# Kernel optimization log

Hardware: AMD Instinct MI355X
Metric: run time of the kernel (lower is better)

The kernel has to match this reference:

```python
import jax, jax.numpy as jnp
import numpy as np

N = 100000      # nodes
E = 1600000     # edges (before self-loops)
IN = 128        # in_dim
HID = 128       # hidden_dim
H = 4           # heads
D = HID // H    # head_dim = 32
L = 3           # n_layers
G = 128         # graphs in batch
NEG_SLOPE = 0.2 # PyG GATConv default leaky_relu slope
BN_EPS = 1e-5


def setup_inputs() -> dict:
    key = jax.random.key(0)
    ks = jax.random.split(key, 16)
    x = jax.random.normal(ks[0], (N, IN), dtype=jnp.float32)
    edge_index = jax.random.randint(ks[1], (2, E), 0, N, dtype=jnp.int64)
    batch = jnp.sort(jax.random.randint(ks[2], (N,), 0, G, dtype=jnp.int64))
    # stacked per-layer GATConv params (in_dim == hidden_dim so all layers stack)
    W = jax.random.normal(ks[3], (L, HID, HID), dtype=jnp.float32) * (1.0 / np.sqrt(HID))
    att_src = jax.random.normal(ks[4], (L, H, D), dtype=jnp.float32) * 0.1
    att_dst = jax.random.normal(ks[5], (L, H, D), dtype=jnp.float32) * 0.1
    bias = jax.random.normal(ks[6], (L, HID), dtype=jnp.float32) * 0.01
    # BatchNorm1d (eval mode: running stats)
    gamma = 1.0 + 0.1 * jax.random.normal(ks[7], (L, HID), dtype=jnp.float32)
    beta = 0.01 * jax.random.normal(ks[8], (L, HID), dtype=jnp.float32)
    bn_mean = jnp.zeros((L, HID), dtype=jnp.float32)
    bn_var = jnp.ones((L, HID), dtype=jnp.float32)
    # MLP head: Linear(HID, HID//2) -> ReLU -> Linear(HID//2, 1)
    Wh1 = jax.random.normal(ks[9], (HID, HID // 2), dtype=jnp.float32) * (1.0 / np.sqrt(HID))
    bh1 = jnp.zeros((HID // 2,), dtype=jnp.float32)
    Wh2 = jax.random.normal(ks[10], (HID // 2, 1), dtype=jnp.float32) * (1.0 / np.sqrt(HID // 2))
    bh2 = jnp.zeros((1,), dtype=jnp.float32)
    return {"x": x, "edge_index": edge_index, "batch": batch, "W": W,
            "att_src": att_src, "att_dst": att_dst, "bias": bias,
            "gamma": gamma, "beta": beta, "bn_mean": bn_mean, "bn_var": bn_var,
            "Wh1": Wh1, "bh1": bh1, "Wh2": Wh2, "bh2": bh2}


def _gat_conv(x, src, dst, W_l, asrc, adst, b):
    # x: [N, F_in]; src/dst: [E+N] (self-loops included); returns [N, H*D]
    h = (x @ W_l).reshape(N, H, D)                      # [N,H,D]
    a_s = jnp.einsum('nhd,hd->nh', h, asrc)             # [N,H]
    a_d = jnp.einsum('nhd,hd->nh', h, adst)
    e = jax.nn.leaky_relu(a_s[src] + a_d[dst], NEG_SLOPE)  # [Etot,H]
    # segment softmax over incoming edges per destination node
    e_max = jax.ops.segment_max(e, dst, num_segments=N)    # [N,H]
    p = jnp.exp(e - e_max[dst])
    denom = jax.ops.segment_sum(p, dst, num_segments=N)    # [N,H]
    alpha = p / (denom[dst] + 1e-16)                        # [Etot,H]
    msg = h[src] * alpha[:, :, None]                        # [Etot,H,D]
    out = jax.ops.segment_sum(msg, dst, num_segments=N)     # [N,H,D]
    return out.reshape(N, H * D) + b


def reference(x, edge_index, batch, W, att_src, att_dst, bias,
              gamma, beta, bn_mean, bn_var, Wh1, bh1, Wh2, bh2):
    # add self-loops once (PyG GATConv default add_self_loops=True)
    loop = jnp.arange(N, dtype=edge_index.dtype)
    src = jnp.concatenate([edge_index[0], loop])
    dst = jnp.concatenate([edge_index[1], loop])
    for l in range(L):
        x = _gat_conv(x, src, dst, W[l], att_src[l], att_dst[l], bias[l])
        x = jnp.maximum(x, 0.0)
        # BatchNorm1d, eval mode (dropout is identity in eval)
        x = (x - bn_mean[l]) * (gamma[l] / jnp.sqrt(bn_var[l] + BN_EPS)) + beta[l]
    # global mean pool over graphs
    sums = jax.ops.segment_sum(x, batch, num_segments=G)            # [G,HID]
    cnts = jax.ops.segment_sum(jnp.ones((N,), x.dtype), batch, num_segments=G)
    pooled = sums / jnp.maximum(cnts, 1.0)[:, None]
    hdn = jnp.maximum(pooled @ Wh1 + bh1, 0.0)
    return (hdn @ Wh2 + bh2).squeeze(-1)                            # [G]
```

## Files before the change

### kernel.cpp

```cpp
#include <hip/hip_runtime.h>
#include <hip/hip_fp16.h>


typedef __bf16 bf16x8 __attribute__((ext_vector_type(8)));
typedef float  f32x4  __attribute__((ext_vector_type(4)));
typedef unsigned int u32x4 __attribute__((ext_vector_type(4)));

#define BCOLS 144
#define BSTRIDE (BCOLS * 128)

#define MAXBKT 800
#define BCAP   4096

__global__ __launch_bounds__(256)
void k_bucket(const int* __restrict__ ei, unsigned int* __restrict__ bkt,
              int* __restrict__ bcnt, float* __restrict__ gsum,
              int* __restrict__ gcnt, int Ne, int Nn, int nbkt, int Gg) {
    __shared__ int lcnt[MAXBKT];
    __shared__ int lbase[MAXBKT];
    int tid = threadIdx.x;
    int gid = blockIdx.x * 256 + tid;
    if (gid < Gg * 128) gsum[gid] = 0.f;
    if (gid < Gg) gcnt[gid] = 0;
    for (int i = tid; i < nbkt; i += 256) lcnt[i] = 0;
    __syncthreads();
    int chunk0 = blockIdx.x * 2048;
    int nnz = Ne + Nn;
    for (int i = 0; i < 8; ++i) {
        int e = chunk0 + i * 256 + tid;
        if (e < nnz) {
            int d = (e < Ne) ? ei[Ne + e] : (e - Ne);
            atomicAdd(&lcnt[d >> 7], 1);
        }
    }
    __syncthreads();
    for (int b = tid; b < nbkt; b += 256) {
        int c = lcnt[b];
        lbase[b] = (c > 0) ? atomicAdd(&bcnt[b], c) : 0;
        lcnt[b] = 0;
    }
    __syncthreads();
    for (int i = 0; i < 8; ++i) {
        int e = chunk0 + i * 256 + tid;
        if (e < nnz) {
            int s, d;
            if (e < Ne) { s = ei[e]; d = ei[Ne + e]; }
            else        { s = e - Ne; d = e - Ne; }
            int b = d >> 7;
            int r = atomicAdd(&lcnt[b], 1);
            bkt[(long)b * BCAP + lbase[b] + r] = ((unsigned)s << 7) | (unsigned)(d & 127);
        }
    }
}

__global__ __launch_bounds__(1024)
void k_bktscan(const int* __restrict__ bcnt, int* __restrict__ bktbase, int nbkt) {
    __shared__ int s0[1024], s1[1024];
    int t = threadIdx.x;
    int v = (t < nbkt) ? bcnt[t] : 0;
    s0[t] = v;
    __syncthreads();
    int* src = s0; int* dst = s1;
    for (int off = 1; off < 1024; off <<= 1) {
        int x = src[t];
        if (t >= off) x += src[t - off];
        dst[t] = x;
        __syncthreads();
        int* tw = src; src = dst; dst = tw;
    }
    if (t < nbkt) bktbase[t] = src[t] - v;
}

__global__ __launch_bounds__(256)
void k_bscatter2(const unsigned int* __restrict__ bkt, const int* __restrict__ bcnt,
                 const int* __restrict__ bktbase, int* __restrict__ rowptr,
                 int* __restrict__ colv, int Nn, int nnz) {
    __shared__ int h[128], sc0[128], sc1[128];
    int b = blockIdx.x;
    int tid = threadIdx.x;
    if (tid < 128) h[tid] = 0;
    __syncthreads();
    int cnt = bcnt[b];
    int base = bktbase[b];
    const unsigned int* bp = bkt + (long)b * BCAP;
    for (int i = tid; i < cnt; i += 256) atomicAdd(&h[bp[i] & 127], 1);
    __syncthreads();
    if (tid < 128) sc0[tid] = h[tid];
    __syncthreads();
    int* src = sc0; int* dst = sc1;
    for (int off = 1; off < 128; off <<= 1) {
        if (tid < 128) {
            int x = src[tid];
            if (tid >= off) x += src[tid - off];
            dst[tid] = x;
        }
        __syncthreads();
        int* tw = src; src = dst; dst = tw;
    }
    int node = b * 128 + tid;
    if (tid < 128) {
        int excl = src[tid] - h[tid];
        int st = base + excl;
        h[tid] = st;
        if (node < Nn) rowptr[node] = st;
    }
    if (b == 0 && tid == 0) rowptr[Nn] = nnz;
    __syncthreads();
    for (int i = tid; i < cnt; i += 256) {
        unsigned int e = bp[i];
        int pos = atomicAdd(&h[e & 127], 1);
        colv[pos] = (int)(e >> 7);
    }
}

__global__ void k_prep(const float* __restrict__ gamma, const float* __restrict__ beta,
                       const float* __restrict__ mean, const float* __restrict__ var,
                       float* __restrict__ bn_mul, float* __restrict__ bn_add,
                       const float* __restrict__ W, const float* __restrict__ asrc,
                       const float* __restrict__ adst,
                       __bf16* __restrict__ Hi, __bf16* __restrict__ Lo) {
    int gid = blockIdx.x * 256 + threadIdx.x;
    if (gid < 384) {
        float sc = gamma[gid] / sqrtf(var[gid] + 1e-5f);
        bn_mul[gid] = sc;
        bn_add[gid] = beta[gid] - mean[gid] * sc;
    }
    if (gid < 3 * 128 * 128) {
        int l = gid >> 14;
        int k = (gid >> 7) & 127;
        int n = gid & 127;
        float f = W[gid];
        __bf16 h = (__bf16)f;
        int o = l * BSTRIDE + n * 128 + k;
        Hi[o] = h;
        Lo[o] = (__bf16)(f - (float)h);
    }
    if (gid < 3 * 128 * 8) {
        int l = gid >> 10;
        int r = gid & 1023;
        int k = r >> 3;
        int j = r & 7;
        int hh = j & 3;
        const float* av = (j < 4 ? asrc : adst) + l * 128 + hh * 32;
        const float* wp = W + l * 16384 + k * 128 + hh * 32;
        float sum = 0.f;
#pragma unroll
        for (int d = 0; d < 32; ++d) sum = fmaf(wp[d], av[d], sum);
        __bf16 h = (__bf16)sum;
        int o = l * BSTRIDE + (128 + j) * 128 + k;
        Hi[o] = h;
        Lo[o] = (__bf16)(sum - (float)h);
    }
    if (gid < 3 * 128 * 8) {
        int l = gid >> 10;
        int r = gid & 1023;
        int k = r >> 3;
        int j = r & 7;
        int o = l * BSTRIDE + (136 + j) * 128 + k;
        Hi[o] = (__bf16)0.f;
        Lo[o] = (__bf16)0.f;
    }
}

__global__ __launch_bounds__(256)
void k_gemm_mfma(const float* __restrict__ X, const __bf16* __restrict__ BtHi,
                 const __bf16* __restrict__ BtLo, __half* __restrict__ Hout,
                 float* __restrict__ as_, float* __restrict__ ad_, int Nn) {
    __shared__ __bf16 sB[18 * 512];
    int t = threadIdx.x;
    int w = t >> 6;
    int lane = t & 63;
    int li = lane & 15;
    int b  = lane >> 4;
    long rowBase = (long)blockIdx.x * 128 + w * 32;

    f32x4 acc[2][9];
#pragma unroll
    for (int rt = 0; rt < 2; ++rt)
#pragma unroll
        for (int ct = 0; ct < 9; ++ct) acc[rt][ct] = (f32x4){0.f, 0.f, 0.f, 0.f};

    long rA[2];
#pragma unroll
    for (int rt = 0; rt < 2; ++rt) {
        long r = rowBase + rt * 16 + li;
        rA[rt] = (r > Nn - 1) ? (Nn - 1) : r;
    }
    const __bf16* Bt[2] = {BtHi, BtLo};

    for (int ks = 0; ks < 4; ++ks) {
        if (ks) __syncthreads();
#pragma unroll
        for (int tile = w; tile < 18; tile += 4) {
            int d = (tile >= 9) ? 1 : 0;
            int ct = tile - d * 9;
            bf16x8 v = *(const bf16x8*)(Bt[d] + (ct * 16 + li) * 128 + ks * 32 + b * 8);
            *(bf16x8*)(sB + tile * 512 + lane * 8) = v;
        }
        __syncthreads();

        int k0 = ks * 32 + 8 * b;
        bf16x8 ahi[2], alo[2];
#pragma unroll
        for (int rt = 0; rt < 2; ++rt) {
            const float* xp = X + rA[rt] * 128 + k0;
            float4 f0 = *(const float4*)xp;
            float4 f1 = *(const float4*)(xp + 4);
            float af[8] = {f0.x, f0.y, f0.z, f0.w, f1.x, f1.y, f1.z, f1.w};
#pragma unroll
            for (int j = 0; j < 8; ++j) {
                __bf16 h = (__bf16)af[j];
                ahi[rt][j] = h;
                alo[rt][j] = (__bf16)(af[j] - (float)h);
            }
        }
#pragma unroll
        for (int ct = 0; ct < 9; ++ct) {
            bf16x8 bhi = *(const bf16x8*)(sB + ct * 512 + lane * 8);
            bf16x8 blo = *(const bf16x8*)(sB + (9 + ct) * 512 + lane * 8);
#pragma unroll
            for (int rt = 0; rt < 2; ++rt) {
                acc[rt][ct] = __builtin_amdgcn_mfma_f32_16x16x32_bf16(bhi, ahi[rt], acc[rt][ct], 0, 0, 0);
                acc[rt][ct] = __builtin_amdgcn_mfma_f32_16x16x32_bf16(bhi, alo[rt], acc[rt][ct], 0, 0, 0);
                acc[rt][ct] = __builtin_amdgcn_mfma_f32_16x16x32_bf16(blo, ahi[rt], acc[rt][ct], 0, 0, 0);
            }
        }
    }

#pragma unroll
    for (int rt = 0; rt < 2; ++rt) {
        long r = rowBase + rt * 16 + li;
        if (r < Nn) {
            __half* op = Hout + r * 128 + 4 * b;
#pragma unroll
            for (int ct = 0; ct < 8; ++ct) {
                union { __half2 h2[2]; uint2 u; } pk;
                pk.h2[0] = __floats2half2_rn(acc[rt][ct][0], acc[rt][ct][1]);
                pk.h2[1] = __floats2half2_rn(acc[rt][ct][2], acc[rt][ct][3]);
                *(uint2*)(op + ct * 16) = pk.u;
            }
            if (b == 0)
                *(float4*)(as_ + 4 * r) = make_float4(acc[rt][8][0], acc[rt][8][1],
                                                      acc[rt][8][2], acc[rt][8][3]);
            else if (b == 1)
                *(float4*)(ad_ + 4 * r) = make_float4(acc[rt][8][0], acc[rt][8][1],
                                                      acc[rt][8][2], acc[rt][8][3]);
        }
    }
}

#define LEAKY(x) ((x) > 0.f ? (x) : 0.2f * (x))

__global__ __launch_bounds__(256)
void k_aggregate(const __half* __restrict__ Hb, const float* __restrict__ as_,
                 const float* __restrict__ ad_, const int* __restrict__ rowptr,
                 const int* __restrict__ col, const float* __restrict__ bias,
                 const float* __restrict__ bn_mul, const float* __restrict__ bn_add,
                 float* __restrict__ Xout, int Nn) {
    __shared__ int2 s_pk[4][64][4];
    int w = threadIdx.x >> 6;
    int n = (blockIdx.x << 2) + w;
    if (n >= Nn) return;
    int lane = threadIdx.x & 63;
    int start = rowptr[n], end = rowptr[n + 1];
    int deg = end - start;

    if (deg <= 64) {
        int hh = lane & 3;
        int slot = lane >> 2;
        float adn = ad_[4 * n + hh];
        float esc[4]; int scl[4];
#pragma unroll
        for (int c = 0; c < 4; ++c) {
            int eidx = (c << 4) + slot;
            float e = -1e30f; int s = 0;
            if (eidx < deg) {
                s = col[start + eidx];
                e = LEAKY(as_[4 * s + hh] + adn);
            }
            esc[c] = e; scl[c] = s;
        }
        float m = fmaxf(fmaxf(esc[0], esc[1]), fmaxf(esc[2], esc[3]));
#pragma unroll
        for (int msk = 4; msk < 64; msk <<= 1) m = fmaxf(m, __shfl_xor(m, msk, 64));
        float p[4];
        float den = 0.f;
#pragma unroll
        for (int c = 0; c < 4; ++c) { p[c] = __expf(esc[c] - m); den += p[c]; }
#pragma unroll
        for (int msk = 4; msk < 64; msk <<= 1) den += __shfl_xor(den, msk, 64);
        float inv = 1.f / (den + 1e-16f);
#pragma unroll
        for (int c = 0; c < 4; ++c) {
            int2 pk;
            pk.x = scl[c] << 8;
            pk.y = __float_as_int(p[c] * inv);
            s_pk[w][(c << 4) + slot][hh] = pk;
        }

        int quarter = lane >> 4;
        int li = lane & 15;
        int hB = li >> 2;
        int cByte = li << 4;
        const char* hb8 = (const char*)Hb;
        float acc[8];
#pragma unroll
        for (int i = 0; i < 8; ++i) acc[i] = 0.f;

        int nit = (deg + 7) >> 3;
        int2 pk0 = s_pk[w][quarter][hB];
        int2 pk1 = s_pk[w][quarter + 4][hB];
        float a0 = __int_as_float(pk0.y);
        float a1 = __int_as_float(pk1.y);
        u32x4 r0 = *(const u32x4*)(hb8 + pk0.x + cByte);
        u32x4 r1 = *(const u32x4*)(hb8 + pk1.x + cByte);
        for (int it = 1; it < nit; ++it) {
            int e0 = (it << 3) + quarter;
            int2 q0 = s_pk[w][e0][hB];
            int2 q1 = s_pk[w][e0 + 4][hB];
            u32x4 t0 = *(const u32x4*)(hb8 + q0.x + cByte);
            u32x4 t1 = *(const u32x4*)(hb8 + q1.x + cByte);
            const __half* h0 = (const __half*)&r0;
            const __half* h1 = (const __half*)&r1;
#pragma unroll
            for (int q = 0; q < 8; ++q) {
                acc[q] = fmaf(__half2float(h0[q]), a0, acc[q]);
                acc[q] = fmaf(__half2float(h1[q]), a1, acc[q]);
            }
            r0 = t0; r1 = t1;
            a0 = __int_as_float(q0.y);
            a1 = __int_as_float(q1.y);
        }
        {
            const __half* h0 = (const __half*)&r0;
            const __half* h1 = (const __half*)&r1;
#pragma unroll
            for (int q = 0; q < 8; ++q) {
                acc[q] = fmaf(__half2float(h0[q]), a0, acc[q]);
                acc[q] = fmaf(__half2float(h1[q]), a1, acc[q]);
            }
        }
#pragma unroll
        for (int i = 0; i < 8; ++i) {
            float v = acc[i];
            v += __shfl_xor(v, 16, 64);
            v += __shfl_xor(v, 32, 64);
            acc[i] = v;
        }
        if (lane < 16) {
            int c0 = li << 3;
            float4 bz0 = *(const float4*)(bias + c0);
            float4 bz1 = *(const float4*)(bias + c0 + 4);
            float4 m0 = *(const float4*)(bn_mul + c0);
            float4 m1 = *(const float4*)(bn_mul + c0 + 4);
            float4 a0v = *(const float4*)(bn_add + c0);
            float4 a1v = *(const float4*)(bn_add + c0 + 4);
            float4 o0, o1;
            o0.x = fmaf(fmaxf(acc[0] + bz0.x, 0.f), m0.x, a0v.x);
            o0.y = fmaf(fmaxf(acc[1] + bz0.y, 0.f), m0.y, a0v.y);
            o0.z = fmaf(fmaxf(acc[2] + bz0.z, 0.f), m0.z, a0v.z);
            o0.w = fmaf(fmaxf(acc[3] + bz0.w, 0.f), m0.w, a0v.w);
            o1.x = fmaf(fmaxf(acc[4] + bz1.x, 0.f), m1.x, a1v.x);
            o1.y = fmaf(fmaxf(acc[5] + bz1.y, 0.f), m1.y, a1v.y);
            o1.z = fmaf(fmaxf(acc[6] + bz1.z, 0.f), m1.z, a1v.z);
            o1.w = fmaf(fmaxf(acc[7] + bz1.w, 0.f), m1.w, a1v.w);
            *(float4*)(Xout + (long)n * 128 + c0)     = o0;
            *(float4*)(Xout + (long)n * 128 + c0 + 4) = o1;
        }
        return;
    }

    int hh = lane & 3;
    float adn = ad_[n * 4 + hh];
    float m = -1e30f;
    for (int base = start; base < end; base += 16) {
        int idx = base + (lane >> 2);
        float sc = -1e30f;
        if (idx < end) {
            int s = col[idx];
            float e = as_[s * 4 + hh] + adn;
            sc = LEAKY(e);
        }
        m = fmaxf(m, sc);
    }
    for (int msk = 4; msk < 64; msk <<= 1) m = fmaxf(m, __shfl_xor(m, msk, 64));
    float den = 0.f;
    for (int base = start; base < end; base += 16) {
        int idx = base + (lane >> 2);
        if (idx < end) {
            int s = col[idx];
            float e = as_[s * 4 + hh] + adn;
            e = LEAKY(e);
            den += __expf(e - m);
        }
    }
    for (int msk = 4; msk < 64; msk <<= 1) den += __shfl_xor(den, msk, 64);
    int hB = lane >> 4;
    float mB   = __shfl(m, hB, 64);
    float invB = 1.f / (__shfl(den, hB, 64) + 1e-16f);
    float adB  = ad_[n * 4 + hB];
    int c0 = lane << 1;
    float acc0 = 0.f, acc1 = 0.f;
    for (int i = start; i < end; ++i) {
        int s = col[i];
        float e = as_[s * 4 + hB] + adB;
        e = LEAKY(e);
        float alpha = __expf(e - mB) * invB;
        float2 hv = __half22float2(*(const __half2*)(Hb + (long)s * 128 + c0));
        acc0 = fmaf(hv.x, alpha, acc0);
        acc1 = fmaf(hv.y, alpha, acc1);
    }
    float v0 = acc0 + bias[c0], v1 = acc1 + bias[c0 + 1];
    v0 = fmaxf(v0, 0.f); v1 = fmaxf(v1, 0.f);
    v0 = fmaf(v0, bn_mul[c0], bn_add[c0]);
    v1 = fmaf(v1, bn_mul[c0 + 1], bn_add[c0 + 1]);
    *(float2*)(Xout + (long)n * 128 + c0) = make_float2(v0, v1);
}

__global__ __launch_bounds__(128)
void k_pool(const float* __restrict__ X, const int* __restrict__ batch,
            float* __restrict__ gsum, int* __restrict__ gcnt, int Nn) {
    int c = threadIdx.x;
    int n0 = blockIdx.x * 64;
    if (n0 >= Nn) return;
    int nend = (n0 + 64 < Nn) ? n0 + 64 : Nn;
    float local = 0.f;
    int gcur = batch[n0];
    int cnt = 0;
    for (int n = n0; n < nend; ++n) {
        int g = batch[n];
        if (g != gcur) {
            atomicAdd(&gsum[gcur * 128 + c], local);
            if (c == 0) atomicAdd(&gcnt[gcur], cnt);
            local = 0.f; cnt = 0; gcur = g;
        }
        local += X[(long)n * 128 + c];
        cnt += 1;
    }
    atomicAdd(&gsum[gcur * 128 + c], local);
    if (c == 0) atomicAdd(&gcnt[gcur], cnt);
}

__global__ __launch_bounds__(64)
void k_head(const float* __restrict__ gsum, const int* __restrict__ gcnt,
            const float* __restrict__ Wh1, const float* __restrict__ bh1,
            const float* __restrict__ Wh2, const float* __restrict__ bh2,
            float* __restrict__ outp) {
    __shared__ float pooled[128];
    int g = blockIdx.x;
    int j = threadIdx.x;
    int cnt = gcnt[g];
    float inv = 1.f / (float)(cnt > 1 ? cnt : 1);
    pooled[j]      = gsum[g * 128 + j] * inv;
    pooled[j + 64] = gsum[g * 128 + 64 + j] * inv;
    __syncthreads();
    float acc = bh1[j];
    for (int k = 0; k < 128; ++k) acc = fmaf(pooled[k], Wh1[k * 64 + j], acc);
    acc = fmaxf(acc, 0.f);
    float prod = acc * Wh2[j];
    for (int msk = 1; msk < 64; msk <<= 1) prod += __shfl_xor(prod, msk, 64);
    if (j == 0) outp[g] = prod + bh2[0];
}

extern "C" void kernel_launch(void* const* d_in, const int* in_sizes, int n_in,
                              void* d_out, int out_size, void* d_ws, size_t ws_size,
                              hipStream_t stream) {
    const float* x       = (const float*)d_in[0];
    const int*   ei      = (const int*)d_in[1];
    const int*   batch   = (const int*)d_in[2];
    const float* W       = (const float*)d_in[3];
    const float* att_src = (const float*)d_in[4];
    const float* att_dst = (const float*)d_in[5];
    const float* bias    = (const float*)d_in[6];
    const float* gamma   = (const float*)d_in[7];
    const float* beta    = (const float*)d_in[8];
    const float* bn_mean = (const float*)d_in[9];
    const float* bn_var  = (const float*)d_in[10];
    const float* Wh1     = (const float*)d_in[11];
    const float* bh1     = (const float*)d_in[12];
    const float* Wh2     = (const float*)d_in[13];
    const float* bh2     = (const float*)d_in[14];
    float* out = (float*)d_out;

    const int Nn = in_sizes[0] / 128;
    const int Ne = in_sizes[1] / 2;
    const int Gg = out_size;
    const int nnz = Ne + Nn;
    const int nbkt = (Nn + 127) / 128;

    char* ws = (char*)d_ws;
    size_t off = 0;
    auto alloc = [&](size_t bytes) -> char* {
        char* p = ws + off;
        off = (off + bytes + 255) & ~(size_t)255;
        return p;
    };
    float*        bufA    = (float*)alloc((size_t)Nn * 128 * 4);
    __half*       bufH    = (__half*)alloc((size_t)Nn * 128 * 2);
    float*        as_     = (float*)alloc((size_t)Nn * 4 * 4);
    float*        ad_     = (float*)alloc((size_t)Nn * 4 * 4);
    int*          rowptr  = (int*)alloc((size_t)(Nn + 1) * 4);
    int*          col     = (int*)alloc((size_t)nnz * 4);
    float*        bn_mul  = (float*)alloc(384 * 4);
    float*        bn_add  = (float*)alloc(384 * 4);
    float*        gsum    = (float*)alloc((size_t)Gg * 128 * 4);
    int*          gcnt    = (int*)alloc((size_t)Gg * 4);
    __bf16*       WtHi    = (__bf16*)alloc((size_t)3 * BSTRIDE * 2);
    __bf16*       WtLo    = (__bf16*)alloc((size_t)3 * BSTRIDE * 2);
    unsigned int* bkt     = (unsigned int*)alloc((size_t)nbkt * BCAP * 4);
    int*          bcnt    = (int*)alloc((size_t)nbkt * 4);
    int*          bktbase = (int*)alloc((size_t)nbkt * 4);

    hipMemsetAsync(bcnt, 0, (size_t)nbkt * 4, stream);
    k_prep<<<192, 256, 0, stream>>>(gamma, beta, bn_mean, bn_var, bn_mul, bn_add,
                                    W, att_src, att_dst, WtHi, WtLo);
    k_bucket<<<(nnz + 2047) / 2048, 256, 0, stream>>>(ei, bkt, bcnt, gsum, gcnt,
                                                      Ne, Nn, nbkt, Gg);
    k_bktscan<<<1, 1024, 0, stream>>>(bcnt, bktbase, nbkt);
    k_bscatter2<<<nbkt, 256, 0, stream>>>(bkt, bcnt, bktbase, rowptr, col, Nn, nnz);

    const float* cur = x;
    for (int l = 0; l < 3; ++l) {
        k_gemm_mfma<<<(Nn + 127) / 128, 256, 0, stream>>>(cur, WtHi + l * BSTRIDE,
                                                          WtLo + l * BSTRIDE,
                                                          bufH, as_, ad_, Nn);
        k_aggregate<<<(Nn + 3) / 4, 256, 0, stream>>>(bufH, as_, ad_, rowptr, col,
                                                      bias + l * 128, bn_mul + l * 128,
                                                      bn_add + l * 128, bufA, Nn);
        cur = bufA;
    }

    k_pool<<<(Nn + 63) / 64, 128, 0, stream>>>(bufA, batch, gsum, gcnt, Nn);
    k_head<<<Gg, 64, 0, stream>>>(gsum, gcnt, Wh1, bh1, Wh2, bh2, out);
}
```

Before: 528.1 us.

## Issue neighbor feature gathers before softmax and triple-buffer aggregation loads

In the small-degree aggregation path, the gathers of neighbor feature rows for the first three edge chunks are now issued directly from the column indices, before the attention softmax is computed. This hides gather latency behind the softmax work. The main loop becomes a fully unrolled, triple-buffered load/compute chain in place of the single-stage prefetch loop. Shared memory now holds only attention weights instead of packed index/weight pairs, so column indices are re-read from global memory and more registers are used for three in-flight buffers.

```diff
diff --git a/kernel.cpp b/kernel.cpp
--- a/kernel.cpp
+++ b/kernel.cpp
@@ -251,13 +251,37 @@
 
 #define LEAKY(x) ((x) > 0.f ? (x) : 0.2f * (x))
 
+
+#define LOADS(RA, RB, s) {                                                     \
+    int e0 = ((s) << 3) + quarter;                                             \
+    if (e0 + 4 < deg) {                                                        \
+        RA = *(const u32x4*)(hb8 + (col[start + e0] << 8) + cByte);            \
+        RB = *(const u32x4*)(hb8 + (col[start + e0 + 4] << 8) + cByte);        \
+    } else {                                                                   \
+        RA = (u32x4){0u, 0u, 0u, 0u};                                          \
+        RB = (u32x4){0u, 0u, 0u, 0u};                                          \
+        if (e0 < deg)                                                          \
+            RA = *(const u32x4*)(hb8 + (col[start + e0] << 8) + cByte);        \
+    } }
+
+#define COMP(RA, RB, s) {                                                      \
+    float a0 = s_al[w][((s) << 3) + quarter][hB];                              \
+    float a1 = s_al[w][((s) << 3) + quarter + 4][hB];                          \
+    const __half* h0 = (const __half*)&RA;                                     \
+    const __half* h1 = (const __half*)&RB;                                     \
+    _Pragma("unroll")                                                          \
+    for (int q = 0; q < 8; ++q) {                                              \
+        acc[q] = fmaf(__half2float(h0[q]), a0, acc[q]);                        \
+        acc[q] = fmaf(__half2float(h1[q]), a1, acc[q]);                        \
+    } }
+
 __global__ __launch_bounds__(256)
 void k_aggregate(const __half* __restrict__ Hb, const float* __restrict__ as_,
                  const float* __restrict__ ad_, const int* __restrict__ rowptr,
                  const int* __restrict__ col, const float* __restrict__ bias,
                  const float* __restrict__ bn_mul, const float* __restrict__ bn_add,
                  float* __restrict__ Xout, int Nn) {
-    __shared__ int2 s_pk[4][64][4];
+    __shared__ float s_al[4][64][4];
     int w = threadIdx.x >> 6;
     int n = (blockIdx.x << 2) + w;
     if (n >= Nn) return;
@@ -266,80 +290,77 @@
     int deg = end - start;
 
     if (deg <= 64) {
-        int hh = lane & 3;
-        int slot = lane >> 2;
-        float adn = ad_[4 * n + hh];
-        float esc[4]; int scl[4];
-#pragma unroll
-        for (int c = 0; c < 4; ++c) {
-            int eidx = (c << 4) + slot;
-            float e = -1e30f; int s = 0;
-            if (eidx < deg) {
-                s = col[start + eidx];
-                e = LEAKY(as_[4 * s + hh] + adn);
-            }
-            esc[c] = e; scl[c] = s;
-        }
-        float m = fmaxf(fmaxf(esc[0], esc[1]), fmaxf(esc[2], esc[3]));
-#pragma unroll
-        for (int msk = 4; msk < 64; msk <<= 1) m = fmaxf(m, __shfl_xor(m, msk, 64));
-        float p[4];
-        float den = 0.f;
-#pragma unroll
-        for (int c = 0; c < 4; ++c) { p[c] = __expf(esc[c] - m); den += p[c]; }
-#pragma unroll
-        for (int msk = 4; msk < 64; msk <<= 1) den += __shfl_xor(den, msk, 64);
-        float inv = 1.f / (den + 1e-16f);
-#pragma unroll
-        for (int c = 0; c < 4; ++c) {
-            int2 pk;
-            pk.x = scl[c] << 8;
-            pk.y = __float_as_int(p[c] * inv);
-            s_pk[w][(c << 4) + slot][hh] = pk;
-        }
-
         int quarter = lane >> 4;
         int li = lane & 15;
         int hB = li >> 2;
         int cByte = li << 4;
         const char* hb8 = (const char*)Hb;
+        int nit = (deg + 7) >> 3;
+        u32x4 ra0, rb0, ra1, rb1, ra2, rb2;
+        LOADS(ra0, rb0, 0)
+        if (nit > 1) LOADS(ra1, rb1, 1)
+        if (nit > 2) LOADS(ra2, rb2, 2)
+
+        int hh = lane & 3;
+        int slot = lane >> 2;
+        float adn = ad_[4 * n + hh];
+        float esc[4];
+#pragma unroll
+        for (int c = 0; c < 4; ++c) {
+            int eidx = (c << 4) + slot;
+            float e = -1e30f;
+            if (eidx < deg) {
+                int s = col[start + eidx];
+                e = LEAKY(as_[4 * s + hh] + adn);
+            }
+            esc[c] = e;
+        }
+        float m = fmaxf(fmaxf(esc[0], esc[1]), fmaxf(esc[2], esc[3]));
+#pragma unroll
+        for (int msk = 4; msk < 64; msk <<= 1) m = fmaxf(m, __shfl_xor(m, msk, 64));
+        float p[4];
+        float den = 0.f;
+#pragma unroll
+        for (int c = 0; c < 4; ++c) { p[c] = __expf(esc[c] - m); den += p[c]; }
+#pragma unroll
+        for (int msk = 4; msk < 64; msk <<= 1) den += __shfl_xor(den, msk, 64);
+        float inv = 1.f / (den + 1e-16f);
+#pragma unroll
+        for (int c = 0; c < 4; ++c)
+            s_al[w][(c << 4) + slot][hh] = p[c] * inv;
+
         float acc[8];
 #pragma unroll
         for (int i = 0; i < 8; ++i) acc[i] = 0.f;
 
-        int nit = (deg + 7) >> 3;
-        int2 pk0 = s_pk[w][quarter][hB];
-        int2 pk1 = s_pk[w][quarter + 4][hB];
-        float a0 = __int_as_float(pk0.y);
-        float a1 = __int_as_float(pk1.y);
-        u32x4 r0 = *(const u32x4*)(hb8 + pk0.x + cByte);
-        u32x4 r1 = *(const u32x4*)(hb8 + pk1.x + cByte);
-        for (int it = 1; it < nit; ++it) {
-            int e0 = (it << 3) + quarter;
-            int2 q0 = s_pk[w][e0][hB];
-            int2 q1 = s_pk[w][e0 + 4][hB];
-            u32x4 t0 = *(const u32x4*)(hb8 + q0.x + cByte);
-            u32x4 t1 = *(const u32x4*)(hb8 + q1.x + cByte);
-            const __half* h0 = (const __half*)&r0;
-            const __half* h1 = (const __half*)&r1;
-#pragma unroll
-            for (int q = 0; q < 8; ++q) {
-                acc[q] = fmaf(__half2float(h0[q]), a0, acc[q]);
-                acc[q] = fmaf(__half2float(h1[q]), a1, acc[q]);
+        COMP(ra0, rb0, 0)
+        if (nit > 1) {
+            if (nit > 3) LOADS(ra0, rb0, 3)
+            COMP(ra1, rb1, 1)
+            if (nit > 2) {
+                if (nit > 4) LOADS(ra1, rb1, 4)
+                COMP(ra2, rb2, 2)
+                if (nit > 3) {
+                    if (nit > 5) LOADS(ra2, rb2, 5)
+                    COMP(ra0, rb0, 3)
+                    if (nit > 4) {
+                        if (nit > 6) LOADS(ra0, rb0, 6)
+                        COMP(ra1, rb1, 4)
+                        if (nit > 5) {
+                            if (nit > 7) LOADS(ra1, rb1, 7)
+                            COMP(ra2, rb2, 5)
+                            if (nit > 6) {
+                                COMP(ra0, rb0, 6)
+                                if (nit > 7) {
+                                    COMP(ra1, rb1, 7)
+                                }
+                            }
+                        }
+                    }
+                }
             }
-            r0 = t0; r1 = t1;
-            a0 = __int_as_float(q0.y);
-            a1 = __int_as_float(q1.y);
-        }
-        {
-            const __half* h0 = (const __half*)&r0;
-            const __half* h1 = (const __half*)&r1;
-#pragma unroll
-            for (int q = 0; q < 8; ++q) {
-                acc[q] = fmaf(__half2float(h0[q]), a0, acc[q]);
-                acc[q] = fmaf(__half2float(h1[q]), a1, acc[q]);
-            }
-        }
+        }
+
 #pragma unroll
         for (int i = 0; i < 8; ++i) {
             float v = acc[i];
```

Result: slower. 541.2 us (+2.5%).

## Pre-swizzle weights into MFMA fragment order and read B directly from global

Applied to the files above, without the earlier changes.

Weight hi/lo bf16 splits are stored in one buffer laid out in exact MFMA fragment order, so each lane reads its B fragment with one contiguous 16-byte load from global/L2. This removes the shared-memory staging of B and both block barriers per k-step in the GEMM, and fully unrolls the k loop. The cost is that each wave now fetches the weight fragments itself through the cache hierarchy instead of sharing one copy per block.

```diff
diff --git a/kernel.cpp b/kernel.cpp
--- a/kernel.cpp
+++ b/kernel.cpp
@@ -6,8 +6,7 @@
 typedef float  f32x4  __attribute__((ext_vector_type(4)));
 typedef unsigned int u32x4 __attribute__((ext_vector_type(4)));
 
-#define BCOLS 144
-#define BSTRIDE (BCOLS * 128)
+#define WLSZ 36864
 
 #define MAXBKT 800
 #define BCAP   4096
@@ -113,12 +112,17 @@
     }
 }
 
+__device__ __forceinline__ int foff(int l, int d, int n, int k) {
+    int ct = n >> 4, li = n & 15;
+    int ks = k >> 5, bq = (k >> 3) & 3, j = k & 7;
+    return l * WLSZ + (((ks * 18) + d * 9 + ct) * 64 + (bq << 4) + li) * 8 + j;
+}
+
 __global__ void k_prep(const float* __restrict__ gamma, const float* __restrict__ beta,
                        const float* __restrict__ mean, const float* __restrict__ var,
                        float* __restrict__ bn_mul, float* __restrict__ bn_add,
                        const float* __restrict__ W, const float* __restrict__ asrc,
-                       const float* __restrict__ adst,
-                       __bf16* __restrict__ Hi, __bf16* __restrict__ Lo) {
+                       const float* __restrict__ adst, __bf16* __restrict__ WF) {
     int gid = blockIdx.x * 256 + threadIdx.x;
     if (gid < 384) {
         float sc = gamma[gid] / sqrtf(var[gid] + 1e-5f);
@@ -131,9 +135,8 @@
         int n = gid & 127;
         float f = W[gid];
         __bf16 h = (__bf16)f;
-        int o = l * BSTRIDE + n * 128 + k;
-        Hi[o] = h;
-        Lo[o] = (__bf16)(f - (float)h);
+        WF[foff(l, 0, n, k)] = h;
+        WF[foff(l, 1, n, k)] = (__bf16)(f - (float)h);
     }
     if (gid < 3 * 128 * 8) {
         int l = gid >> 10;
@@ -147,26 +150,23 @@
 #pragma unroll
         for (int d = 0; d < 32; ++d) sum = fmaf(wp[d], av[d], sum);
         __bf16 h = (__bf16)sum;
-        int o = l * BSTRIDE + (128 + j) * 128 + k;
-        Hi[o] = h;
-        Lo[o] = (__bf16)(sum - (float)h);
+        WF[foff(l, 0, 128 + j, k)] = h;
+        WF[foff(l, 1, 128 + j, k)] = (__bf16)(sum - (float)h);
     }
     if (gid < 3 * 128 * 8) {
         int l = gid >> 10;
         int r = gid & 1023;
         int k = r >> 3;
         int j = r & 7;
-        int o = l * BSTRIDE + (136 + j) * 128 + k;
-        Hi[o] = (__bf16)0.f;
-        Lo[o] = (__bf16)0.f;
+        WF[foff(l, 0, 136 + j, k)] = (__bf16)0.f;
+        WF[foff(l, 1, 136 + j, k)] = (__bf16)0.f;
     }
 }
 
 __global__ __launch_bounds__(256)
-void k_gemm_mfma(const float* __restrict__ X, const __bf16* __restrict__ BtHi,
-                 const __bf16* __restrict__ BtLo, __half* __restrict__ Hout,
+void k_gemm_mfma(const float* __restrict__ X, const __bf16* __restrict__ WF,
+                 __half* __restrict__ Hout,
                  float* __restrict__ as_, float* __restrict__ ad_, int Nn) {
-    __shared__ __bf16 sB[18 * 512];
     int t = threadIdx.x;
     int w = t >> 6;
     int lane = t & 63;
@@ -186,19 +186,9 @@
         long r = rowBase + rt * 16 + li;
         rA[rt] = (r > Nn - 1) ? (Nn - 1) : r;
     }
-    const __bf16* Bt[2] = {BtHi, BtLo};
-
+
+#pragma unroll
     for (int ks = 0; ks < 4; ++ks) {
-        if (ks) __syncthreads();
-#pragma unroll
-        for (int tile = w; tile < 18; tile += 4) {
-            int d = (tile >= 9) ? 1 : 0;
-            int ct = tile - d * 9;
-            bf16x8 v = *(const bf16x8*)(Bt[d] + (ct * 16 + li) * 128 + ks * 32 + b * 8);
-            *(bf16x8*)(sB + tile * 512 + lane * 8) = v;
-        }
-        __syncthreads();
-
         int k0 = ks * 32 + 8 * b;
         bf16x8 ahi[2], alo[2];
 #pragma unroll
@@ -214,10 +204,11 @@
                 alo[rt][j] = (__bf16)(af[j] - (float)h);
             }
         }
+        const __bf16* wk = WF + (ks * 18) * 512 + lane * 8;
 #pragma unroll
         for (int ct = 0; ct < 9; ++ct) {
-            bf16x8 bhi = *(const bf16x8*)(sB + ct * 512 + lane * 8);
-            bf16x8 blo = *(const bf16x8*)(sB + (9 + ct) * 512 + lane * 8);
+            bf16x8 bhi = *(const bf16x8*)(wk + ct * 512);
+            bf16x8 blo = *(const bf16x8*)(wk + (9 + ct) * 512);
 #pragma unroll
             for (int rt = 0; rt < 2; ++rt) {
                 acc[rt][ct] = __builtin_amdgcn_mfma_f32_16x16x32_bf16(bhi, ahi[rt], acc[rt][ct], 0, 0, 0);
@@ -505,15 +496,14 @@
     float*        bn_add  = (float*)alloc(384 * 4);
     float*        gsum    = (float*)alloc((size_t)Gg * 128 * 4);
     int*          gcnt    = (int*)alloc((size_t)Gg * 4);
-    __bf16*       WtHi    = (__bf16*)alloc((size_t)3 * BSTRIDE * 2);
-    __bf16*       WtLo    = (__bf16*)alloc((size_t)3 * BSTRIDE * 2);
+    __bf16*       WtF     = (__bf16*)alloc((size_t)3 * WLSZ * 2);
     unsigned int* bkt     = (unsigned int*)alloc((size_t)nbkt * BCAP * 4);
     int*          bcnt    = (int*)alloc((size_t)nbkt * 4);
     int*          bktbase = (int*)alloc((size_t)nbkt * 4);
 
     hipMemsetAsync(bcnt, 0, (size_t)nbkt * 4, stream);
     k_prep<<<192, 256, 0, stream>>>(gamma, beta, bn_mean, bn_var, bn_mul, bn_add,
-                                    W, att_src, att_dst, WtHi, WtLo);
+                                    W, att_src, att_dst, WtF);
     k_bucket<<<(nnz + 2047) / 2048, 256, 0, stream>>>(ei, bkt, bcnt, gsum, gcnt,
                                                       Ne, Nn, nbkt, Gg);
     k_bktscan<<<1, 1024, 0, stream>>>(bcnt, bktbase, nbkt);
@@ -521,8 +511,7 @@
 
     const float* cur = x;
     for (int l = 0; l < 3; ++l) {
-        k_gemm_mfma<<<(Nn + 127) / 128, 256, 0, stream>>>(cur, WtHi + l * BSTRIDE,
-                                                          WtLo + l * BSTRIDE,
+        k_gemm_mfma<<<(Nn + 127) / 128, 256, 0, stream>>>(cur, WtF + l * WLSZ,
                                                           bufH, as_, ad_, Nn);
         k_aggregate<<<(Nn + 3) / 4, 256, 0, stream>>>(bufH, as_, ad_, rowptr, col,
                                                       bias + l * 128, bn_mul + l * 128,
```

Measured after the change: 538.8 us. +2.0%, slower.
